# Performance work log

Hardware: AMD Instinct MI355X
Metric: run time of the kernel (lower is better)

The kernel has to match this reference:

```python
import jax, jax.numpy as jnp
import numpy as np

B, S, V, E, H, NL, DFF = 16, 16, 64, 64, 8, 4, 2048
L = S * V
DH = E // H
NUM_GRIDS = 100
POI_DIM = 8
OV_DIM = 8


def setup_inputs() -> dict:
    key = jax.random.key(0)
    ks = jax.random.split(key, 32)
    sc = 0.05
    inp = {}
    inp['features'] = jax.random.normal(ks[0], (B, S, V, 3), jnp.float32)
    inp['overlap_tag'] = jax.random.randint(ks[1], (B, S, V), 0, 3)
    inp['poi_id'] = jax.random.randint(ks[2], (B, S, V), 0, NUM_GRIDS + 1)
    # embedders
    inp['W_raw'] = jax.random.normal(ks[3], (3, E), jnp.float32) * sc
    inp['b_raw'] = jnp.zeros((E,), jnp.float32)
    inp['pos_tab'] = jax.random.normal(ks[4], (S, E), jnp.float32) * sc
    inp['type_tab'] = jax.random.normal(ks[5], (V, E), jnp.float32) * sc
    inp['poi_tab'] = jax.random.normal(ks[6], (NUM_GRIDS + 1, POI_DIM), jnp.float32) * sc
    inp['overlap_tab'] = jax.random.normal(ks[7], (3, OV_DIM), jnp.float32) * sc
    inp['W_comb'] = jax.random.normal(ks[8], (E + OV_DIM + POI_DIM, E), jnp.float32) * sc
    inp['b_comb'] = jnp.zeros((E,), jnp.float32)
    # transformer layers (stacked over NL)
    inp['Wqkv'] = jax.random.normal(ks[9], (NL, E, 3 * E), jnp.float32) * sc
    inp['bqkv'] = jnp.zeros((NL, 3 * E), jnp.float32)
    inp['Wo'] = jax.random.normal(ks[10], (NL, E, E), jnp.float32) * sc
    inp['bo'] = jnp.zeros((NL, E), jnp.float32)
    inp['ln1_s'] = jnp.ones((NL, E), jnp.float32)
    inp['ln1_b'] = jnp.zeros((NL, E), jnp.float32)
    inp['W1'] = jax.random.normal(ks[11], (NL, E, DFF), jnp.float32) * sc
    inp['b1'] = jnp.zeros((NL, DFF), jnp.float32)
    inp['W2'] = jax.random.normal(ks[12], (NL, DFF, E), jnp.float32) * sc
    inp['b2'] = jnp.zeros((NL, E), jnp.float32)
    inp['ln2_s'] = jnp.ones((NL, E), jnp.float32)
    inp['ln2_b'] = jnp.zeros((NL, E), jnp.float32)
    inp['W_head'] = jax.random.normal(ks[13], (E, 3), jnp.float32) * sc
    inp['b_head'] = jnp.zeros((3,), jnp.float32)
    return inp


def _layer_norm(x, s, b):
    m = x.mean(-1, keepdims=True)
    v = ((x - m) ** 2).mean(-1, keepdims=True)
    return (x - m) / jnp.sqrt(v + 1e-5) * s + b


def _forward(features, overlap_tag, poi_id, W_raw, b_raw, pos_tab, type_tab,
             poi_tab, overlap_tab, W_comb, b_comb, Wqkv, bqkv, Wo, bo,
             ln1_s, ln1_b, W1, b1, W2, b2, ln2_s, ln2_b, W_head, b_head):
    # padding_idx=0 rows are zero (as in nn.Embedding(padding_idx=0))
    poi_tab = poi_tab.at[0].set(0.0)
    overlap_tab = overlap_tab.at[0].set(0.0)

    zero_mask = (features.sum(-1) == 0).reshape(B, L)  # [B, L]
    ov_idx = jnp.maximum(overlap_tag, 0)
    poi_idx = jnp.maximum(poi_id, 0)

    feat_e = features @ W_raw + b_raw                    # [B,S,V,E]
    concat = jnp.concatenate([feat_e, overlap_tab[ov_idx], poi_tab[poi_idx]], axis=-1)
    x = (concat @ W_comb + b_comb).reshape(B, L, E)      # [B,L,E]

    t_idx = jnp.repeat(jnp.arange(S), V)                 # [L]
    v_idx = jnp.tile(jnp.arange(V), S)                   # [L]
    struct_mask = (t_idx[:, None] != t_idx[None, :]) & (v_idx[:, None] != v_idx[None, :])
    full_mask = struct_mask[None] | zero_mask[:, None, :] | zero_mask[:, :, None]  # [B,L,L]
    bias = jnp.where(full_mask, -jnp.inf, 0.0)[:, None, :, :]  # [B,1,L,L]

    x = x + pos_tab[t_idx][None] + type_tab[v_idx][None]

    scale = 1.0 / jnp.sqrt(jnp.asarray(DH, x.dtype))
    for l in range(NL):
        qkv = x @ Wqkv[l] + bqkv[l]                      # [B,L,3E]
        q, k, v = jnp.split(qkv, 3, axis=-1)
        q = q.reshape(B, L, H, DH)
        k = k.reshape(B, L, H, DH)
        v = v.reshape(B, L, H, DH)
        scores = jnp.einsum('bqhd,bkhd->bhqk', q, k) * scale + bias
        attn = jax.nn.softmax(scores, axis=-1)
        o = jnp.einsum('bhqk,bkhd->bqhd', attn, v).reshape(B, L, E)
        x = _layer_norm(x + o @ Wo[l] + bo[l], ln1_s[l], ln1_b[l])
        ff = jax.nn.relu(x @ W1[l] + b1[l]) @ W2[l] + b2[l]
        x = _layer_norm(x + ff, ln2_s[l], ln2_b[l])

    last = x.reshape(B, S, V, E)[:, -1]                  # [B,V,E]
    return last @ W_head + b_head                        # [B,V,3]


def reference(features, overlap_tag, poi_id, W_raw, b_raw, pos_tab, type_tab,
              poi_tab, overlap_tab, W_comb, b_comb, Wqkv, bqkv, Wo, bo,
              ln1_s, ln1_b, W1, b1, W2, b2, ln2_s, ln2_b, W_head, b_head):
    return _forward(features, overlap_tag, poi_id, W_raw, b_raw, pos_tab, type_tab,
                    poi_tab, overlap_tab, W_comb, b_comb, Wqkv, bqkv, Wo, bo,
                    ln1_s, ln1_b, W1, b1, W2, b2, ln2_s, ln2_b, W_head, b_head)
```

## Files before the change

kernel.cpp:

```cpp
#include <hip/hip_runtime.h>
#include <math.h>

#define BB 16
#define SS 16
#define VVV 64
#define EE 64
#define HHH 8
#define NLAYER 4
#define DFF_ 2048
#define LL 1024
#define BL 16384
#define PERL 131072

typedef __attribute__((ext_vector_type(8))) _Float16 half8;
typedef __attribute__((ext_vector_type(4))) _Float16 half4v;
typedef __attribute__((ext_vector_type(2))) _Float16 half2v;
typedef __attribute__((ext_vector_type(4))) float f32x4;

#if defined(__has_builtin)
#if __has_builtin(__builtin_amdgcn_fdot2)
#define HAVE_FDOT2 1
#endif
#endif

#define SW64(m, k)  (((m) << 6) + ((((k) >> 3) ^ ((m) & 7)) << 3) + ((k) & 7))


__global__ __launch_bounds__(256) void k_prep(
    const float* __restrict__ W1, const float* __restrict__ W2,
    const float* __restrict__ Wqkv, const float* __restrict__ Wo,
    const float* __restrict__ Wcomb,
    _Float16* __restrict__ w1f, _Float16* __restrict__ w2f,
    _Float16* __restrict__ wqkvf, _Float16* __restrict__ wof,
    _Float16* __restrict__ wcombt)
{
  __shared__ float t[64 * 65];
  int bx = blockIdx.x;
  int cc = threadIdx.x & 63, rr = threadIdx.x >> 6;

  if (bx >= 272) {
    int r0 = (bx - 272) * 64;
#pragma unroll
    for (int i = 0; i < 16; i++) {
      int r = i * 4 + rr;
      if (r0 + r < 80) t[r * 65 + cc] = Wcomb[(size_t)(r0 + r) * 64 + cc];
    }
    __syncthreads();
#pragma unroll
    for (int i = 0; i < 16; i++) {
      int c = i * 4 + rr;
      if (r0 + c < 80) wcombt[(size_t)cc * 80 + r0 + c] = (_Float16)t[c * 65 + cc];
    }
    return;
  }

  const float* src; _Float16* dst; int astr;
  if (bx < 128) {
    int l = bx >> 5, g = bx & 31;
    src = W1 + (size_t)l * PERL + g * 64; astr = 2048;
    dst = w1f + (size_t)(l * 32 + g) * 4096;
  } else if (bx < 256) {
    int j = bx - 128; int l = j >> 5, g = j & 31;
    src = W2 + (size_t)l * PERL + (size_t)g * 64 * 64; astr = 64;
    dst = w2f + (size_t)(l * 32 + g) * 4096;
  } else if (bx < 268) {
    int j = bx - 256; int l = j / 3, g = j % 3;
    src = Wqkv + (size_t)l * 64 * 192 + g * 64; astr = 192;
    dst = wqkvf + (size_t)(l * 3 + g) * 4096;
  } else {
    int l = bx - 268;
    src = Wo + (size_t)l * 4096; astr = 64;
    dst = wof + (size_t)l * 4096;
  }
#pragma unroll
  for (int i = 0; i < 16; i++) {
    int a = i * 4 + rr;
    t[cc * 65 + a] = src[(size_t)a * astr + cc];
  }
  __syncthreads();
#pragma unroll
  for (int it = 0; it < 2; it++) {
    int c = threadIdx.x + it * 256;
    int frag = c >> 6, lane = c & 63;
    int m = (frag >> 1) * 16 + (lane & 15);
    int k0 = (frag & 1) * 32 + (lane >> 4) * 8;
    const float* tr = &t[m * 65 + k0];
    half8 h;
#pragma unroll
    for (int j = 0; j < 8; j++) h[j] = (_Float16)tr[j];
    *(half8*)&dst[(size_t)c * 8] = h;
  }
}

__device__ __forceinline__ void qkv_nb(
    const half8 (&af)[2][2], const _Float16* __restrict__ wqkvf,
    const float* __restrict__ bqkv, _Float16* __restrict__ qbuf,
    _Float16* __restrict__ kbuf, _Float16* __restrict__ vbuf,
    int bx, int nb, int wm, int wn, int lane)
{
  int quad = lane >> 4, l15 = lane & 15;
  const _Float16* bt = wqkvf + (size_t)nb * 4096;
  half8 bf[2][2];
#pragma unroll
  for (int nt = 0; nt < 2; nt++)
#pragma unroll
    for (int ks = 0; ks < 2; ks++)
      bf[nt][ks] = *(const half8*)&bt[(size_t)(((wn * 2 + nt) * 2 + ks) * 512) +
                                      lane * 8];
  f32x4 acc[2][2];
#pragma unroll
  for (int mt = 0; mt < 2; mt++)
#pragma unroll
    for (int nt = 0; nt < 2; nt++) {
      float bv = bqkv[nb * 64 + wn * 32 + nt * 16 + l15];
      acc[mt][nt] = (f32x4){bv, bv, bv, bv};
    }
#pragma unroll
  for (int ks = 0; ks < 2; ks++)
#pragma unroll
    for (int mt = 0; mt < 2; mt++)
#pragma unroll
      for (int nt = 0; nt < 2; nt++)
        acc[mt][nt] = __builtin_amdgcn_mfma_f32_16x16x32_f16(
            af[mt][ks], bf[nt][ks], acc[mt][nt], 0, 0, 0);
  _Float16* dst = (nb == 0) ? qbuf : ((nb == 1) ? kbuf : vbuf);
#pragma unroll
  for (int mt = 0; mt < 2; mt++)
#pragma unroll
    for (int nt = 0; nt < 2; nt++) {
      int col = wn * 32 + nt * 16 + l15;
      int h = col >> 3, d = col & 7;
#pragma unroll
      for (int r = 0; r < 4; r++) {
        int row = bx * 64 + wm * 32 + mt * 16 + quad * 4 + r;
        int b = row >> 10, rb = row & 1023;
        dst[((size_t)(b * 8 + h) * 1024 + rb) * 8 + d] = (_Float16)acc[mt][nt][r];
      }
    }
}

__device__ __forceinline__ void ffn_load2(
    const _Float16* __restrict__ w1f, const _Float16* __restrict__ w2f, int g,
    half8 (&a1)[2][2], half8 (&b2w)[2][2], int wn, int lane)
{
  const _Float16* w1t_ = w1f + (size_t)g * 4096;
  const _Float16* w2t_ = w2f + (size_t)g * 4096;
#pragma unroll
  for (int ht = 0; ht < 2; ht++)
#pragma unroll
    for (int ks = 0; ks < 2; ks++)
      a1[ht][ks] = *(const half8*)&w1t_[(size_t)(((wn * 2 + ht) * 2 + ks) * 512) +
                                        lane * 8];
#pragma unroll
  for (int nt = 0; nt < 2; nt++)
#pragma unroll
    for (int ks = 0; ks < 2; ks++)
      b2w[nt][ks] = *(const half8*)&w2t_[(size_t)(((wn * 2 + nt) * 2 + ks) * 512) +
                                         lane * 8];
}

__device__ __forceinline__ void ffn_step2(
    const half8 (&a1)[2][2], const half8 (&b2w)[2][2], const half8 (&xb)[2][2],
    _Float16* hsbuf, const float* __restrict__ b1, int g, f32x4 (&acc)[2][2],
    int wn, int lane)
{
  int quad = lane >> 4, l15 = lane & 15;
  f32x4 hacc[2][2];
#pragma unroll
  for (int ht = 0; ht < 2; ht++)
#pragma unroll
    for (int mt = 0; mt < 2; mt++) hacc[ht][mt] = (f32x4){0.f, 0.f, 0.f, 0.f};
#pragma unroll
  for (int ks = 0; ks < 2; ks++)
#pragma unroll
    for (int ht = 0; ht < 2; ht++)
#pragma unroll
      for (int mt = 0; mt < 2; mt++)
        hacc[ht][mt] = __builtin_amdgcn_mfma_f32_16x16x32_f16(
            a1[ht][ks], xb[mt][ks], hacc[ht][mt], 0, 0, 0);
#pragma unroll
  for (int ht = 0; ht < 2; ht++) {
    float4 bb = *(const float4*)&b1[g * 64 + wn * 32 + ht * 16 + quad * 4];
#pragma unroll
    for (int mt = 0; mt < 2; mt++) {
      f32x4 hv = hacc[ht][mt];
      half4v hp = (half4v){
          (_Float16)fmaxf(hv[0] + bb.x, 0.f), (_Float16)fmaxf(hv[1] + bb.y, 0.f),
          (_Float16)fmaxf(hv[2] + bb.z, 0.f), (_Float16)fmaxf(hv[3] + bb.w, 0.f)};
      *(half4v*)&hsbuf[SW64(mt * 16 + l15, wn * 32 + ht * 16 + quad * 4)] = hp;
    }
  }
  __syncthreads();
#pragma unroll
  for (int ks = 0; ks < 2; ks++)
#pragma unroll
    for (int mt = 0; mt < 2; mt++) {
      half8 a2 = *(const half8*)&hsbuf[SW64(mt * 16 + l15, ks * 32 + quad * 8)];
#pragma unroll
      for (int nt = 0; nt < 2; nt++)
        acc[mt][nt] = __builtin_amdgcn_mfma_f32_16x16x32_f16(a2, b2w[nt][ks],
                                                             acc[mt][nt], 0, 0, 0);
    }
}

__global__ __launch_bounds__(256) void k_embqkv(
    const float* __restrict__ features, const int* __restrict__ ovtag,
    const int* __restrict__ poiid, const float* __restrict__ W_raw,
    const float* __restrict__ b_raw, const float* __restrict__ ov_tab,
    const float* __restrict__ poi_tab, const _Float16* __restrict__ wcombt,
    const float* __restrict__ b_comb, const float* __restrict__ pos_tab,
    const float* __restrict__ type_tab, float* __restrict__ x1,
    float* __restrict__ zm, const _Float16* __restrict__ wqkvf,
    const float* __restrict__ bqkv, _Float16* __restrict__ qbuf,
    _Float16* __restrict__ kbuf, _Float16* __restrict__ vbuf)
{
  constexpr int KP = 104;
  __shared__ _Float16 As[64 * KP];
  __shared__ _Float16 Bs[64 * KP];
  __shared__ _Float16 xs[4096];
  int tid = threadIdx.x;
  int raw = blockIdx.x;
  int bx = ((raw & 7) << 5) + (raw >> 3);
  int m0 = bx * 64;
  int wave = tid >> 6, lane = tid & 63, quad = lane >> 4, l15 = lane & 15;
  int wm = wave >> 1, wn = wave & 1;
  for (int p = tid; p < 1536; p += 256) {
    int r = p / 24, s = p - r * 24; int c = s * 4;
    int row = m0 + r;
    float f0 = features[row * 3 + 0];
    float f1 = features[row * 3 + 1];
    float f2 = features[row * 3 + 2];
    if (s == 0) zm[row] = ((f0 + f1 + f2) == 0.f) ? 1.f : 0.f;
    half4v h;
#pragma unroll
    for (int j = 0; j < 4; j++) {
      int cc = c + j; float v;
      if (cc < 64) {
        v = b_raw[cc] + f0 * W_raw[cc] + f1 * W_raw[64 + cc] + f2 * W_raw[128 + cc];
      } else if (cc < 72) {
        int tt = ovtag[row]; v = (tt <= 0) ? 0.f : ov_tab[tt * 8 + cc - 64];
      } else if (cc < 80) {
        int tt = poiid[row]; v = (tt <= 0) ? 0.f : poi_tab[tt * 8 + cc - 72];
      } else v = 0.f;
      h[j] = (_Float16)v;
    }
    *(half4v*)&As[r * KP + c] = h;
  }
  for (int p = tid; p < 1536; p += 256) {
    int r = p / 24, s = p - r * 24; int c = s * 4;
    half4v h = (half4v){0, 0, 0, 0};
    if (c < 80) h = *(const half4v*)&wcombt[r * 80 + c];
    *(half4v*)&Bs[r * KP + c] = h;
  }
  __syncthreads();
  f32x4 acc[2][2];
#pragma unroll
  for (int mt = 0; mt < 2; mt++)
#pragma unroll
    for (int nt = 0; nt < 2; nt++) {
      float bv = b_comb[wn * 32 + nt * 16 + l15];
      acc[mt][nt] = (f32x4){bv, bv, bv, bv};
    }
#pragma unroll
  for (int ks = 0; ks < 3; ks++) {
    half8 af[2], bf[2];
#pragma unroll
    for (int mt = 0; mt < 2; mt++)
      af[mt] = *(const half8*)&As[(wm * 32 + mt * 16 + l15) * KP + ks * 32 + quad * 8];
#pragma unroll
    for (int nt = 0; nt < 2; nt++)
      bf[nt] = *(const half8*)&Bs[(wn * 32 + nt * 16 + l15) * KP + ks * 32 + quad * 8];
#pragma unroll
    for (int mt = 0; mt < 2; mt++)
#pragma unroll
      for (int nt = 0; nt < 2; nt++)
        acc[mt][nt] = __builtin_amdgcn_mfma_f32_16x16x32_f16(af[mt], bf[nt],
                                                             acc[mt][nt], 0, 0, 0);
  }
#pragma unroll
  for (int mt = 0; mt < 2; mt++)
#pragma unroll
    for (int nt = 0; nt < 2; nt++)
#pragma unroll
      for (int r = 0; r < 4; r++) {
        int lrow = wm * 32 + mt * 16 + quad * 4 + r;
        int row = m0 + lrow;
        int col = wn * 32 + nt * 16 + l15;
        int l = row & (LL - 1);
        float v = acc[mt][nt][r] +
            pos_tab[(l >> 6) * 64 + col] + type_tab[(l & 63) * 64 + col];
        x1[(size_t)row * 64 + col] = v;
        xs[SW64(lrow, col)] = (_Float16)v;
      }
  __syncthreads();
  half8 af[2][2];
#pragma unroll
  for (int mt = 0; mt < 2; mt++)
#pragma unroll
    for (int ks = 0; ks < 2; ks++)
      af[mt][ks] = *(const half8*)&xs[SW64(wm * 32 + mt * 16 + l15,
                                           ks * 32 + quad * 8)];
  for (int nb = 0; nb < 3; nb++)
    qkv_nb(af, wqkvf, bqkv, qbuf, kbuf, vbuf, bx, nb, wm, wn, lane);
}

__global__ __launch_bounds__(256, 2) void k_layerf(
    const _Float16* __restrict__ qin, const _Float16* __restrict__ kin,
    const _Float16* __restrict__ vin, const float* __restrict__ zm,
    const _Float16* __restrict__ wof, const float* __restrict__ bo,
    float* __restrict__ x1,
    const float* __restrict__ ln1_s, const float* __restrict__ ln1_b,
    const _Float16* __restrict__ w1f, const _Float16* __restrict__ w2f,
    const float* __restrict__ b1, const float* __restrict__ b2,
    const float* __restrict__ ln2_s, const float* __restrict__ ln2_b,
    const _Float16* __restrict__ wqkvf, const float* __restrict__ bqkv,
    _Float16* __restrict__ qout, _Float16* __restrict__ kout,
    _Float16* __restrict__ vout, int doqkv,
    const float* __restrict__ Wh, const float* __restrict__ bh,
    float* __restrict__ out)
{
  __shared__ float ots[32 * 68];
  __shared__ __align__(16) _Float16 xs[2048];
  __shared__ float x2f[2048];
  __shared__ __align__(16) _Float16 hs[4][2048];
  __shared__ __align__(16) _Float16 os[2048];
  __shared__ float zsh[1024];
  __shared__ __align__(16) _Float16 kvs[8192];
  __shared__ float ots2[32 * 68];
  int tid = threadIdx.x;
  int raw = blockIdx.x;
  int bx = ((raw & 7) << 6) + (raw >> 3);
  int r0 = bx * 32;
  int rb0 = r0 & 1023;
  int wave = tid >> 6, lane = tid & 63;
  int quad = lane >> 4, l15 = lane & 15;
  int grp = wave >> 1, wn = wave & 1;
  int b = r0 >> 10;
  int tq0 = rb0 >> 6;

  for (int p = tid; p < 1024; p += 256)
    zsh[p] = (zm[b * LL + p] != 0.f) ? -20000.f : 0.f;
  for (int p = tid; p < 512; p += 256) {
    int h = p >> 6, row = p & 63;
    size_t gidx = ((size_t)(b * 8 + h) * 1024 + tq0 * 64 + row) * 8;
    *(half8*)&kvs[h * 512 + row * 8] = *(const half8*)&kin[gidx];
    *(half8*)&kvs[4096 + h * 512 + row * 8] = *(const half8*)&vin[gidx];
  }

  half8 obf[2][2];
#pragma unroll
  for (int nt = 0; nt < 2; nt++)
#pragma unroll
    for (int ks = 0; ks < 2; ks++)
      obf[nt][ks] = *(const half8*)&wof[(size_t)(((wn * 2 + nt) * 2 + ks) * 512) +
                                        lane * 8];
  float x1pre[8];
#pragma unroll
  for (int i = 0; i < 8; i++)
    x1pre[i] = x1[(size_t)(r0 + wave * 8 + i) * 64 + lane];
  float ln1sv = ln1_s[lane], ln1bv = ln1_b[lane];
  float ln2sv = ln2_s[lane], ln2bv = ln2_b[lane];
  float fb2 = b2[lane];
  __syncthreads();

  {
    int lr = tid & 31, hh = tid >> 5;
    int rb = rb0 + lr;
    int vq = rb & 63;
    const _Float16* kb = kin + (size_t)(b * 8 + hh) * 8192;
    const _Float16* vb = vin + (size_t)(b * 8 + hh) * 8192;
    half8 qh = *(const half8*)&qin[(size_t)(b * 8 + hh) * 8192 + (size_t)rb * 8];
    const float scale = 0.3535533905932738f;
    float m = -10000.f, lsum = 0.f;
    float acc[8] = {0.f, 0.f, 0.f, 0.f, 0.f, 0.f, 0.f, 0.f};
    bool zmq = (zsh[rb] < -1.f);

    auto dot = [&](half8 kk) -> float {
      float s = 0.f;
#ifdef HAVE_FDOT2
#pragma unroll
      for (int j = 0; j < 4; j++) {
        half2v qa = (half2v){qh[2 * j], qh[2 * j + 1]};
        half2v ka = (half2v){kk[2 * j], kk[2 * j + 1]};
        s = __builtin_amdgcn_fdot2(qa, ka, s, false);
      }
#else
#pragma unroll
      for (int j = 0; j < 8; j++) s += (float)qh[j] * (float)kk[j];
#endif
      return s;
    };
    auto update = [&](float s, half8 vv) {
      float nm = fmaxf(m, s);
      float r = __expf(m - nm);
      float p = __expf(s - nm);
      lsum = lsum * r + p;
#pragma unroll
      for (int d = 0; d < 8; d++) acc[d] = acc[d] * r + p * (float)vv[d];
      m = nm;
    };

    if (!zmq) {
      for (int base = 0; base < 64; base += 4) {
        half8 kk[4], vv[4]; float sv[4];
#pragma unroll
        for (int j = 0; j < 4; j++) {
          kk[j] = *(const half8*)&kvs[hh * 512 + (base + j) * 8];
          vv[j] = *(const half8*)&kvs[4096 + hh * 512 + (base + j) * 8];
        }
#pragma unroll
        for (int j = 0; j < 4; j++)
          sv[j] = dot(kk[j]) * scale + zsh[tq0 * 64 + base + j];
#pragma unroll
        for (int j = 0; j < 4; j++) update(sv[j], vv[j]);
      }
      for (int bb = 0; bb < 5; bb++) {
        half8 kk[3], vv[3]; float sv[3];
#pragma unroll
        for (int j = 0; j < 3; j++) {
          int cc = bb * 3 + j;
          int tt = cc + ((cc >= tq0) ? 1 : 0);
          int k = tt * 64 + vq;
          kk[j] = *(const half8*)&kb[(size_t)k * 8];
          vv[j] = *(const half8*)&vb[(size_t)k * 8];
          sv[j] = zsh[k];
        }
#pragma unroll
        for (int j = 0; j < 3; j++) sv[j] += dot(kk[j]) * scale;
#pragma unroll
        for (int j = 0; j < 3; j++) update(sv[j], vv[j]);
      }
    }
    float inv = (lsum > 0.f) ? 1.f / lsum : 0.f;
    half8 o;
#pragma unroll
    for (int d = 0; d < 8; d++) o[d] = (_Float16)(acc[d] * inv);
    *(half8*)&os[SW64(lr, hh * 8)] = o;
  }
  __syncthreads();

  {
    half8 af[2];
#pragma unroll
    for (int ks = 0; ks < 2; ks++)
      af[ks] = *(const half8*)&os[SW64(grp * 16 + l15, ks * 32 + quad * 8)];
    f32x4 acc[2];
#pragma unroll
    for (int nt = 0; nt < 2; nt++) {
      float bv = bo[wn * 32 + nt * 16 + l15];
      acc[nt] = (f32x4){bv, bv, bv, bv};
    }
#pragma unroll
    for (int ks = 0; ks < 2; ks++)
#pragma unroll
      for (int nt = 0; nt < 2; nt++)
        acc[nt] = __builtin_amdgcn_mfma_f32_16x16x32_f16(af[ks], obf[nt][ks],
                                                         acc[nt], 0, 0, 0);
#pragma unroll
    for (int nt = 0; nt < 2; nt++)
#pragma unroll
      for (int r = 0; r < 4; r++)
        ots[(grp * 16 + quad * 4 + r) * 68 + wn * 32 + nt * 16 + l15] = acc[nt][r];
  }
  half8 a1x[2][2], b2x[2][2], a1y[2][2], b2y[2][2];
  ffn_load2(w1f, w2f, grp, a1x, b2x, wn, lane);
  __syncthreads();
  for (int i = 0; i < 8; i++) {
    int row = wave * 8 + i;
    float val = ots[row * 68 + lane] + x1pre[i];
    float sum = val;
#pragma unroll
    for (int o = 32; o > 0; o >>= 1) sum += __shfl_xor(sum, o);
    float mean = sum * (1.f / 64.f);
    float d = val - mean;
    float sq = d * d;
#pragma unroll
    for (int o = 32; o > 0; o >>= 1) sq += __shfl_xor(sq, o);
    float xv = d * rsqrtf(sq * (1.f / 64.f) + 1e-5f) * ln1sv + ln1bv;
    x2f[row * 64 + lane] = xv;
    xs[SW64(row, lane)] = (_Float16)xv;
  }
  __syncthreads();

  half8 xb[2][2];
#pragma unroll
  for (int mt = 0; mt < 2; mt++)
#pragma unroll
    for (int ks = 0; ks < 2; ks++)
      xb[mt][ks] = *(const half8*)&xs[SW64(mt * 16 + l15, ks * 32 + quad * 8)];
  f32x4 acc[2][2];
#pragma unroll
  for (int mt = 0; mt < 2; mt++)
#pragma unroll
    for (int nt = 0; nt < 2; nt++) {
      float bv = (grp == 0) ? b2[wn * 32 + nt * 16 + l15] : 0.f;
      acc[mt][nt] = (f32x4){bv, bv, bv, bv};
    }
  for (int ii = 0; ii < 8; ii++) {
    ffn_load2(w1f, w2f, ii * 4 + 2 + grp, a1y, b2y, wn, lane);
    ffn_step2(a1x, b2x, xb, &hs[grp][0], b1, ii * 4 + grp, acc, wn, lane);
    if (ii < 7) ffn_load2(w1f, w2f, ii * 4 + 4 + grp, a1x, b2x, wn, lane);
    ffn_step2(a1y, b2y, xb, &hs[grp + 2][0], b1, ii * 4 + 2 + grp, acc, wn, lane);
  }
  __syncthreads();
  if (grp == 0) {
#pragma unroll
    for (int mt = 0; mt < 2; mt++)
#pragma unroll
      for (int nt = 0; nt < 2; nt++)
#pragma unroll
        for (int r = 0; r < 4; r++)
          ots[(mt * 16 + quad * 4 + r) * 68 + wn * 32 + nt * 16 + l15] =
              acc[mt][nt][r];
  }
  __syncthreads();
  if (grp == 1) {
#pragma unroll
    for (int mt = 0; mt < 2; mt++)
#pragma unroll
      for (int nt = 0; nt < 2; nt++)
#pragma unroll
        for (int r = 0; r < 4; r++)
          ots[(mt * 16 + quad * 4 + r) * 68 + wn * 32 + nt * 16 + l15] +=
              acc[mt][nt][r];
  }
  __syncthreads();
  for (int i = 0; i < 8; i++) {
    int row = wave * 8 + i;
    size_t off = (size_t)(r0 + row) * 64 + lane;
    float val = ots[row * 68 + lane] + x2f[row * 64 + lane];
    float sum = val;
#pragma unroll
    for (int o = 32; o > 0; o >>= 1) sum += __shfl_xor(sum, o);
    float mean = sum * (1.f / 64.f);
    float d = val - mean;
    float sq = d * d;
#pragma unroll
    for (int o = 32; o > 0; o >>= 1) sq += __shfl_xor(sq, o);
    float xv = d * rsqrtf(sq * (1.f / 64.f) + 1e-5f) * ln2sv + ln2bv;
    x1[off] = xv;
    x2f[row * 64 + lane] = xv;
    xs[SW64(row, lane)] = (_Float16)xv;
  }
  if (!doqkv) {
    __syncthreads();
    if ((bx & 31) >= 30 && tid < 96) {
      int bb2 = bx >> 5;
      int i = tid / 3, j = tid - i * 3;
      int vglob = (bx & 1) * 32 + i;
      float a = bh[j];
      for (int e = 0; e < 64; e++)
        a += x2f[i * 64 + e] * Wh[e * 3 + j];
      out[((size_t)(bb2 * 64 + vglob)) * 3 + j] = a;
    }
    return;
  }
  __syncthreads();
  half8 af[2][2];
#pragma unroll
  for (int mt = 0; mt < 2; mt++)
#pragma unroll
    for (int ks = 0; ks < 2; ks++)
      af[mt][ks] = *(const half8*)&xs[SW64(mt * 16 + l15, ks * 32 + quad * 8)];
  for (int nb = 0; nb < 3; nb++) {
    const _Float16* bt = wqkvf + (size_t)nb * 4096;
    half8 bf[2];
#pragma unroll
    for (int ks = 0; ks < 2; ks++)
      bf[ks] = *(const half8*)&bt[(size_t)((wave * 2 + ks) * 512) + lane * 8];
    f32x4 qacc[2];
#pragma unroll
    for (int mt = 0; mt < 2; mt++) {
      float bv = bqkv[nb * 64 + wave * 16 + l15];
      qacc[mt] = (f32x4){bv, bv, bv, bv};
    }
#pragma unroll
    for (int ks = 0; ks < 2; ks++)
#pragma unroll
      for (int mt = 0; mt < 2; mt++)
        qacc[mt] = __builtin_amdgcn_mfma_f32_16x16x32_f16(af[mt][ks], bf[ks],
                                                          qacc[mt], 0, 0, 0);
    _Float16* dst = (nb == 0) ? qout : ((nb == 1) ? kout : vout);
    int col = wave * 16 + l15;
    int h2 = col >> 3, d2 = col & 7;
#pragma unroll
    for (int mt = 0; mt < 2; mt++)
#pragma unroll
      for (int r = 0; r < 4; r++) {
        int row = r0 + mt * 16 + quad * 4 + r;
        int rbq = row & 1023;
        dst[((size_t)(b * 8 + h2) * 1024 + rbq) * 8 + d2] = (_Float16)qacc[mt][r];
      }
  }
}

extern "C" void kernel_launch(void* const* d_in, const int* in_sizes, int n_in,
                              void* d_out, int out_size, void* d_ws, size_t ws_size,
                              hipStream_t stream) {
  const float* features = (const float*)d_in[0];
  const int*   ovtag    = (const int*)d_in[1];
  const int*   poiid    = (const int*)d_in[2];
  const float* W_raw    = (const float*)d_in[3];
  const float* b_raw    = (const float*)d_in[4];
  const float* pos_tab  = (const float*)d_in[5];
  const float* type_tab = (const float*)d_in[6];
  const float* poi_tab  = (const float*)d_in[7];
  const float* ov_tab   = (const float*)d_in[8];
  const float* W_comb   = (const float*)d_in[9];
  const float* b_comb   = (const float*)d_in[10];
  const float* Wqkv     = (const float*)d_in[11];
  const float* bqkv     = (const float*)d_in[12];
  const float* Wo       = (const float*)d_in[13];
  const float* bo       = (const float*)d_in[14];
  const float* ln1_s    = (const float*)d_in[15];
  const float* ln1_b    = (const float*)d_in[16];
  const float* W1       = (const float*)d_in[17];
  const float* b1       = (const float*)d_in[18];
  const float* W2       = (const float*)d_in[19];
  const float* b2       = (const float*)d_in[20];
  const float* ln2_s    = (const float*)d_in[21];
  const float* ln2_b    = (const float*)d_in[22];
  const float* W_head   = (const float*)d_in[23];
  const float* b_head   = (const float*)d_in[24];
  float* out = (float*)d_out;
  float* ws  = (float*)d_ws;

  float* zm  = ws;
  float* x1  = zm + BL;
  _Float16* qbA = (_Float16*)(x1 + (size_t)BL * 64);
  _Float16* kbA = qbA + (size_t)BL * 64;
  _Float16* vbA = kbA + (size_t)BL * 64;
  _Float16* qbB = vbA + (size_t)BL * 64;
  _Float16* kbB = qbB + (size_t)BL * 64;
  _Float16* vbB = kbB + (size_t)BL * 64;
  _Float16* wcombt = vbB + (size_t)BL * 64;
  _Float16* w1f    = wcombt + 5120;
  _Float16* w2f    = w1f + (size_t)NLAYER * PERL;
  _Float16* wqkvf  = w2f + (size_t)NLAYER * PERL;
  _Float16* wof    = wqkvf + (size_t)NLAYER * 3 * 4096;

  k_prep<<<274, 256, 0, stream>>>(W1, W2, Wqkv, Wo, W_comb,
                                  w1f, w2f, wqkvf, wof, wcombt);
  k_embqkv<<<256, 256, 0, stream>>>(features, ovtag, poiid, W_raw, b_raw,
                                    ov_tab, poi_tab, wcombt, b_comb,
                                    pos_tab, type_tab, x1, zm,
                                    wqkvf, bqkv, qbA, kbA, vbA);
  for (int l = 0; l < NLAYER; l++) {
    const _Float16* qin = (l & 1) ? qbB : qbA;
    const _Float16* kin = (l & 1) ? kbB : kbA;
    const _Float16* vin = (l & 1) ? vbB : vbA;
    _Float16* qout = (l & 1) ? qbA : qbB;
    _Float16* kout = (l & 1) ? kbA : kbB;
    _Float16* vout = (l & 1) ? vbA : vbB;
    int doqkv = (l < NLAYER - 1);
    k_layerf<<<512, 256, 0, stream>>>(
        qin, kin, vin, zm,
        wof + (size_t)l * 4096, bo + l * EE, x1,
        ln1_s + l * EE, ln1_b + l * EE,
        w1f + (size_t)l * PERL, w2f + (size_t)l * PERL,
        b1 + l * DFF_, b2 + l * EE,
        ln2_s + l * EE, ln2_b + l * EE,
        wqkvf + (size_t)(l + 1 < NLAYER ? l + 1 : 0) * 3 * 4096,
        bqkv + (l + 1 < NLAYER ? l + 1 : 0) * 192,
        qout, kout, vout, doqkv, W_head, b_head, out);
  }
}
```

Measured before the change: 267.8 us.

## Merge weight prep into embedding kernel, store residual in fp16, hoist FFN weight loads

Combines the weight-preparation kernel and the embedding+QKV kernel into one launch. Weight-repack blocks run beside embedding blocks, which now read W_comb and Wqkv directly from fp32 global memory instead of the repacked buffers. The residual stream x1 is stored in fp16 instead of fp32, which halves its traffic, and the final layer skips that write. The first FFN weight fragments are loaded earlier so their latency overlaps attention. The cost is lower residual precision, plus strided uncached-style global reads for Wqkv in every embedding block.

```diff
diff --git a/kernel.cpp b/kernel.cpp
--- a/kernel.cpp
+++ b/kernel.cpp
@@ -26,119 +26,6 @@
 #define SW64(m, k)  (((m) << 6) + ((((k) >> 3) ^ ((m) & 7)) << 3) + ((k) & 7))
 
 
-__global__ __launch_bounds__(256) void k_prep(
-    const float* __restrict__ W1, const float* __restrict__ W2,
-    const float* __restrict__ Wqkv, const float* __restrict__ Wo,
-    const float* __restrict__ Wcomb,
-    _Float16* __restrict__ w1f, _Float16* __restrict__ w2f,
-    _Float16* __restrict__ wqkvf, _Float16* __restrict__ wof,
-    _Float16* __restrict__ wcombt)
-{
-  __shared__ float t[64 * 65];
-  int bx = blockIdx.x;
-  int cc = threadIdx.x & 63, rr = threadIdx.x >> 6;
-
-  if (bx >= 272) {
-    int r0 = (bx - 272) * 64;
-#pragma unroll
-    for (int i = 0; i < 16; i++) {
-      int r = i * 4 + rr;
-      if (r0 + r < 80) t[r * 65 + cc] = Wcomb[(size_t)(r0 + r) * 64 + cc];
-    }
-    __syncthreads();
-#pragma unroll
-    for (int i = 0; i < 16; i++) {
-      int c = i * 4 + rr;
-      if (r0 + c < 80) wcombt[(size_t)cc * 80 + r0 + c] = (_Float16)t[c * 65 + cc];
-    }
-    return;
-  }
-
-  const float* src; _Float16* dst; int astr;
-  if (bx < 128) {
-    int l = bx >> 5, g = bx & 31;
-    src = W1 + (size_t)l * PERL + g * 64; astr = 2048;
-    dst = w1f + (size_t)(l * 32 + g) * 4096;
-  } else if (bx < 256) {
-    int j = bx - 128; int l = j >> 5, g = j & 31;
-    src = W2 + (size_t)l * PERL + (size_t)g * 64 * 64; astr = 64;
-    dst = w2f + (size_t)(l * 32 + g) * 4096;
-  } else if (bx < 268) {
-    int j = bx - 256; int l = j / 3, g = j % 3;
-    src = Wqkv + (size_t)l * 64 * 192 + g * 64; astr = 192;
-    dst = wqkvf + (size_t)(l * 3 + g) * 4096;
-  } else {
-    int l = bx - 268;
-    src = Wo + (size_t)l * 4096; astr = 64;
-    dst = wof + (size_t)l * 4096;
-  }
-#pragma unroll
-  for (int i = 0; i < 16; i++) {
-    int a = i * 4 + rr;
-    t[cc * 65 + a] = src[(size_t)a * astr + cc];
-  }
-  __syncthreads();
-#pragma unroll
-  for (int it = 0; it < 2; it++) {
-    int c = threadIdx.x + it * 256;
-    int frag = c >> 6, lane = c & 63;
-    int m = (frag >> 1) * 16 + (lane & 15);
-    int k0 = (frag & 1) * 32 + (lane >> 4) * 8;
-    const float* tr = &t[m * 65 + k0];
-    half8 h;
-#pragma unroll
-    for (int j = 0; j < 8; j++) h[j] = (_Float16)tr[j];
-    *(half8*)&dst[(size_t)c * 8] = h;
-  }
-}
-
-__device__ __forceinline__ void qkv_nb(
-    const half8 (&af)[2][2], const _Float16* __restrict__ wqkvf,
-    const float* __restrict__ bqkv, _Float16* __restrict__ qbuf,
-    _Float16* __restrict__ kbuf, _Float16* __restrict__ vbuf,
-    int bx, int nb, int wm, int wn, int lane)
-{
-  int quad = lane >> 4, l15 = lane & 15;
-  const _Float16* bt = wqkvf + (size_t)nb * 4096;
-  half8 bf[2][2];
-#pragma unroll
-  for (int nt = 0; nt < 2; nt++)
-#pragma unroll
-    for (int ks = 0; ks < 2; ks++)
-      bf[nt][ks] = *(const half8*)&bt[(size_t)(((wn * 2 + nt) * 2 + ks) * 512) +
-                                      lane * 8];
-  f32x4 acc[2][2];
-#pragma unroll
-  for (int mt = 0; mt < 2; mt++)
-#pragma unroll
-    for (int nt = 0; nt < 2; nt++) {
-      float bv = bqkv[nb * 64 + wn * 32 + nt * 16 + l15];
-      acc[mt][nt] = (f32x4){bv, bv, bv, bv};
-    }
-#pragma unroll
-  for (int ks = 0; ks < 2; ks++)
-#pragma unroll
-    for (int mt = 0; mt < 2; mt++)
-#pragma unroll
-      for (int nt = 0; nt < 2; nt++)
-        acc[mt][nt] = __builtin_amdgcn_mfma_f32_16x16x32_f16(
-            af[mt][ks], bf[nt][ks], acc[mt][nt], 0, 0, 0);
-  _Float16* dst = (nb == 0) ? qbuf : ((nb == 1) ? kbuf : vbuf);
-#pragma unroll
-  for (int mt = 0; mt < 2; mt++)
-#pragma unroll
-    for (int nt = 0; nt < 2; nt++) {
-      int col = wn * 32 + nt * 16 + l15;
-      int h = col >> 3, d = col & 7;
-#pragma unroll
-      for (int r = 0; r < 4; r++) {
-        int row = bx * 64 + wm * 32 + mt * 16 + quad * 4 + r;
-        int b = row >> 10, rb = row & 1023;
-        dst[((size_t)(b * 8 + h) * 1024 + rb) * 8 + d] = (_Float16)acc[mt][nt][r];
-      }
-    }
-}
-
 __device__ __forceinline__ void ffn_load2(
     const _Float16* __restrict__ w1f, const _Float16* __restrict__ w2f, int g,
     half8 (&a1)[2][2], half8 (&b2w)[2][2], int wn, int lane)
@@ -203,23 +90,72 @@
     }
 }
 
-__global__ __launch_bounds__(256) void k_embqkv(
+__global__ __launch_bounds__(256) void k_prepemb(
+    const float* __restrict__ W1, const float* __restrict__ W2,
+    const float* __restrict__ Wqkv, const float* __restrict__ Wo,
+    const float* __restrict__ Wcomb,
+    _Float16* __restrict__ w1f, _Float16* __restrict__ w2f,
+    _Float16* __restrict__ wqkvf, _Float16* __restrict__ wof,
     const float* __restrict__ features, const int* __restrict__ ovtag,
     const int* __restrict__ poiid, const float* __restrict__ W_raw,
     const float* __restrict__ b_raw, const float* __restrict__ ov_tab,
-    const float* __restrict__ poi_tab, const _Float16* __restrict__ wcombt,
-    const float* __restrict__ b_comb, const float* __restrict__ pos_tab,
-    const float* __restrict__ type_tab, float* __restrict__ x1,
-    float* __restrict__ zm, const _Float16* __restrict__ wqkvf,
+    const float* __restrict__ poi_tab, const float* __restrict__ b_comb,
+    const float* __restrict__ pos_tab, const float* __restrict__ type_tab,
+    _Float16* __restrict__ x1h, float* __restrict__ zm,
     const float* __restrict__ bqkv, _Float16* __restrict__ qbuf,
     _Float16* __restrict__ kbuf, _Float16* __restrict__ vbuf)
 {
+  int gbx = blockIdx.x;
+  int tid = threadIdx.x;
+
+  if (gbx < 272) {
+    __shared__ float t[64 * 65];
+    int bx = gbx;
+    int cc = tid & 63, rr = tid >> 6;
+    const float* src; _Float16* dst; int astr;
+    if (bx < 128) {
+      int l = bx >> 5, g = bx & 31;
+      src = W1 + (size_t)l * PERL + g * 64; astr = 2048;
+      dst = w1f + (size_t)(l * 32 + g) * 4096;
+    } else if (bx < 256) {
+      int j = bx - 128; int l = j >> 5, g = j & 31;
+      src = W2 + (size_t)l * PERL + (size_t)g * 64 * 64; astr = 64;
+      dst = w2f + (size_t)(l * 32 + g) * 4096;
+    } else if (bx < 268) {
+      int j = bx - 256; int l = j / 3, g = j % 3;
+      src = Wqkv + (size_t)l * 64 * 192 + g * 64; astr = 192;
+      dst = wqkvf + (size_t)(l * 3 + g) * 4096;
+    } else {
+      int l = bx - 268;
+      src = Wo + (size_t)l * 4096; astr = 64;
+      dst = wof + (size_t)l * 4096;
+    }
+#pragma unroll
+    for (int i = 0; i < 16; i++) {
+      int a = i * 4 + rr;
+      t[cc * 65 + a] = src[(size_t)a * astr + cc];
+    }
+    __syncthreads();
+#pragma unroll
+    for (int it = 0; it < 2; it++) {
+      int c = tid + it * 256;
+      int frag = c >> 6, lane = c & 63;
+      int m = (frag >> 1) * 16 + (lane & 15);
+      int k0 = (frag & 1) * 32 + (lane >> 4) * 8;
+      const float* tr = &t[m * 65 + k0];
+      half8 h;
+#pragma unroll
+      for (int j = 0; j < 8; j++) h[j] = (_Float16)tr[j];
+      *(half8*)&dst[(size_t)c * 8] = h;
+    }
+    return;
+  }
+
   constexpr int KP = 104;
   __shared__ _Float16 As[64 * KP];
   __shared__ _Float16 Bs[64 * KP];
   __shared__ _Float16 xs[4096];
-  int tid = threadIdx.x;
-  int raw = blockIdx.x;
+  int raw = gbx - 272;
   int bx = ((raw & 7) << 5) + (raw >> 3);
   int m0 = bx * 64;
   int wave = tid >> 6, lane = tid & 63, quad = lane >> 4, l15 = lane & 15;
@@ -249,7 +185,9 @@
   for (int p = tid; p < 1536; p += 256) {
     int r = p / 24, s = p - r * 24; int c = s * 4;
     half4v h = (half4v){0, 0, 0, 0};
-    if (c < 80) h = *(const half4v*)&wcombt[r * 80 + c];
+#pragma unroll
+    for (int j = 0; j < 4; j++)
+      if (c + j < 80) h[j] = (_Float16)Wcomb[(size_t)(c + j) * 64 + r];
     *(half4v*)&Bs[r * KP + c] = h;
   }
   __syncthreads();
@@ -289,7 +227,7 @@
         int l = row & (LL - 1);
         float v = acc[mt][nt][r] +
             pos_tab[(l >> 6) * 64 + col] + type_tab[(l & 63) * 64 + col];
-        x1[(size_t)row * 64 + col] = v;
+        x1h[(size_t)row * 64 + col] = (_Float16)v;
         xs[SW64(lrow, col)] = (_Float16)v;
       }
   __syncthreads();
@@ -300,15 +238,57 @@
     for (int ks = 0; ks < 2; ks++)
       af[mt][ks] = *(const half8*)&xs[SW64(wm * 32 + mt * 16 + l15,
                                            ks * 32 + quad * 8)];
-  for (int nb = 0; nb < 3; nb++)
-    qkv_nb(af, wqkvf, bqkv, qbuf, kbuf, vbuf, bx, nb, wm, wn, lane);
+#pragma unroll
+  for (int nb = 0; nb < 3; nb++) {
+    half8 bf[2][2];
+#pragma unroll
+    for (int nt = 0; nt < 2; nt++)
+#pragma unroll
+      for (int ks = 0; ks < 2; ks++) {
+        int n = nb * 64 + (wn * 2 + nt) * 16 + l15;
+#pragma unroll
+        for (int j = 0; j < 8; j++)
+          bf[nt][ks][j] =
+              (_Float16)Wqkv[(size_t)(ks * 32 + quad * 8 + j) * 192 + n];
+      }
+    f32x4 qacc[2][2];
+#pragma unroll
+    for (int mt = 0; mt < 2; mt++)
+#pragma unroll
+      for (int nt = 0; nt < 2; nt++) {
+        float bv = bqkv[nb * 64 + wn * 32 + nt * 16 + l15];
+        qacc[mt][nt] = (f32x4){bv, bv, bv, bv};
+      }
+#pragma unroll
+    for (int ks = 0; ks < 2; ks++)
+#pragma unroll
+      for (int mt = 0; mt < 2; mt++)
+#pragma unroll
+        for (int nt = 0; nt < 2; nt++)
+          qacc[mt][nt] = __builtin_amdgcn_mfma_f32_16x16x32_f16(
+              af[mt][ks], bf[nt][ks], qacc[mt][nt], 0, 0, 0);
+    _Float16* dst = (nb == 0) ? qbuf : ((nb == 1) ? kbuf : vbuf);
+#pragma unroll
+    for (int mt = 0; mt < 2; mt++)
+#pragma unroll
+      for (int nt = 0; nt < 2; nt++) {
+        int col = wn * 32 + nt * 16 + l15;
+        int h = col >> 3, d = col & 7;
+#pragma unroll
+        for (int r = 0; r < 4; r++) {
+          int row = m0 + wm * 32 + mt * 16 + quad * 4 + r;
+          int b = row >> 10, rb = row & 1023;
+          dst[((size_t)(b * 8 + h) * 1024 + rb) * 8 + d] = (_Float16)qacc[mt][nt][r];
+        }
+      }
+  }
 }
 
 __global__ __launch_bounds__(256, 2) void k_layerf(
     const _Float16* __restrict__ qin, const _Float16* __restrict__ kin,
     const _Float16* __restrict__ vin, const float* __restrict__ zm,
     const _Float16* __restrict__ wof, const float* __restrict__ bo,
-    float* __restrict__ x1,
+    _Float16* __restrict__ x1h,
     const float* __restrict__ ln1_s, const float* __restrict__ ln1_b,
     const _Float16* __restrict__ w1f, const _Float16* __restrict__ w2f,
     const float* __restrict__ b1, const float* __restrict__ b2,
@@ -357,10 +337,11 @@
   float x1pre[8];
 #pragma unroll
   for (int i = 0; i < 8; i++)
-    x1pre[i] = x1[(size_t)(r0 + wave * 8 + i) * 64 + lane];
+    x1pre[i] = (float)x1h[(size_t)(r0 + wave * 8 + i) * 64 + lane];
   float ln1sv = ln1_s[lane], ln1bv = ln1_b[lane];
   float ln2sv = ln2_s[lane], ln2bv = ln2_b[lane];
-  float fb2 = b2[lane];
+  half8 a1x[2][2], b2x[2][2], a1y[2][2], b2y[2][2];
+  ffn_load2(w1f, w2f, grp, a1x, b2x, wn, lane);
   __syncthreads();
 
   {
@@ -462,8 +443,6 @@
       for (int r = 0; r < 4; r++)
         ots[(grp * 16 + quad * 4 + r) * 68 + wn * 32 + nt * 16 + l15] = acc[nt][r];
   }
-  half8 a1x[2][2], b2x[2][2], a1y[2][2], b2y[2][2];
-  ffn_load2(w1f, w2f, grp, a1x, b2x, wn, lane);
   __syncthreads();
   for (int i = 0; i < 8; i++) {
     int row = wave * 8 + i;
@@ -538,7 +517,7 @@
 #pragma unroll
     for (int o = 32; o > 0; o >>= 1) sq += __shfl_xor(sq, o);
     float xv = d * rsqrtf(sq * (1.f / 64.f) + 1e-5f) * ln2sv + ln2bv;
-    x1[off] = xv;
+    if (doqkv) x1h[off] = (_Float16)xv;
     x2f[row * 64 + lane] = xv;
     xs[SW64(row, lane)] = (_Float16)xv;
   }
@@ -626,25 +605,23 @@
   float* ws  = (float*)d_ws;
 
   float* zm  = ws;
-  float* x1  = zm + BL;
-  _Float16* qbA = (_Float16*)(x1 + (size_t)BL * 64);
+  _Float16* x1h = (_Float16*)(zm + BL);
+  _Float16* qbA = x1h + (size_t)BL * 64;
   _Float16* kbA = qbA + (size_t)BL * 64;
   _Float16* vbA = kbA + (size_t)BL * 64;
   _Float16* qbB = vbA + (size_t)BL * 64;
   _Float16* kbB = qbB + (size_t)BL * 64;
   _Float16* vbB = kbB + (size_t)BL * 64;
-  _Float16* wcombt = vbB + (size_t)BL * 64;
-  _Float16* w1f    = wcombt + 5120;
+  _Float16* w1f    = vbB + (size_t)BL * 64;
   _Float16* w2f    = w1f + (size_t)NLAYER * PERL;
   _Float16* wqkvf  = w2f + (size_t)NLAYER * PERL;
   _Float16* wof    = wqkvf + (size_t)NLAYER * 3 * 4096;
 
-  k_prep<<<274, 256, 0, stream>>>(W1, W2, Wqkv, Wo, W_comb,
-                                  w1f, w2f, wqkvf, wof, wcombt);
-  k_embqkv<<<256, 256, 0, stream>>>(features, ovtag, poiid, W_raw, b_raw,
-                                    ov_tab, poi_tab, wcombt, b_comb,
-                                    pos_tab, type_tab, x1, zm,
-                                    wqkvf, bqkv, qbA, kbA, vbA);
+  k_prepemb<<<528, 256, 0, stream>>>(W1, W2, Wqkv, Wo, W_comb,
+                                     w1f, w2f, wqkvf, wof,
+                                     features, ovtag, poiid, W_raw, b_raw,
+                                     ov_tab, poi_tab, b_comb, pos_tab, type_tab,
+                                     x1h, zm, bqkv, qbA, kbA, vbA);
   for (int l = 0; l < NLAYER; l++) {
     const _Float16* qin = (l & 1) ? qbB : qbA;
     const _Float16* kin = (l & 1) ? kbB : kbA;
@@ -655,7 +632,7 @@
     int doqkv = (l < NLAYER - 1);
     k_layerf<<<512, 256, 0, stream>>>(
         qin, kin, vin, zm,
-        wof + (size_t)l * 4096, bo + l * EE, x1,
+        wof + (size_t)l * 4096, bo + l * EE, x1h,
         ln1_s + l * EE, ln1_b + l * EE,
         w1f + (size_t)l * PERL, w2f + (size_t)l * PERL,
         b1 + l * DFF_, b2 + l * EE,
```

After: 273.5 us. 2.1% more time.
